# Kernel tuning notes

Hardware: AMD Instinct MI355X
Metric: run time of the kernel (lower is better)

The kernel has to match this reference:

```python
import jax, jax.numpy as jnp
import numpy as np

SPATIAL_SCALE = 0.125  # stride-8 FPN level
POINTS = 5


def _sample_points(bb):
    # bb: [N,H,W,5] = (cx, cy, w, h, theta) in image coords
    cx, cy, w, h, t = [bb[..., i] for i in range(5)]
    if POINTS == 1:
        px = cx[..., None]
        py = cy[..., None]
    else:
        vx = w * jnp.cos(t) * 0.5
        vy = w * jnp.sin(t) * 0.5
        wx = -h * jnp.sin(t) * 0.5
        wy = h * jnp.cos(t) * 0.5
        px = jnp.stack([cx, cx + vx + wx, cx - vx + wx, cx - vx - wx, cx + vx - wx], axis=-1)
        py = jnp.stack([cy, cy + vy + wy, cy - vy + wy, cy - vy - wy, cy + vy - wy], axis=-1)
    return px * SPATIAL_SCALE, py * SPATIAL_SCALE  # [N,H,W,P] feature-map coords


def _bilinear_gather(feat, y, x):
    # feat: [N,C,H,W]; y,x: [N,H,W,P] -> [N,H,W,P,C], mmcv-style bilinear w/ border rules
    N, C, H, W = feat.shape
    valid = (y >= -1.0) & (y <= H) & (x >= -1.0) & (x <= W)
    y = jnp.maximum(y, 0.0)
    x = jnp.maximum(x, 0.0)
    y_low = jnp.minimum(jnp.floor(y).astype(jnp.int32), H - 1)
    x_low = jnp.minimum(jnp.floor(x).astype(jnp.int32), W - 1)
    # if low index hits last row/col, snap coordinate onto it (ly/lx = 0)
    y = jnp.where(y_low >= H - 1, y_low.astype(feat.dtype), y)
    x = jnp.where(x_low >= W - 1, x_low.astype(feat.dtype), x)
    y_high = jnp.minimum(y_low + 1, H - 1)
    x_high = jnp.minimum(x_low + 1, W - 1)
    ly = y - y_low.astype(feat.dtype)
    lx = x - x_low.astype(feat.dtype)
    hy = 1.0 - ly
    hx = 1.0 - lx
    nn = jnp.arange(N)[:, None, None, None]  # broadcasts against [N,H,W,P]

    def g(yy, xx):
        return feat[nn, :, yy, xx]  # [N,H,W,P,C]

    val = ((hy * hx)[..., None] * g(y_low, x_low)
           + (hy * lx)[..., None] * g(y_low, x_high)
           + (ly * hx)[..., None] * g(y_high, x_low)
           + (ly * lx)[..., None] * g(y_high, x_high))
    return jnp.where(valid[..., None], val, 0.0)


def feature_refine(features, best_rbboxes):
    px, py = _sample_points(best_rbboxes)
    sampled = _bilinear_gather(features, py, px)       # [N,H,W,P,C]
    acc = sampled.sum(axis=3)                           # [N,H,W,C]
    return features + jnp.transpose(acc, (0, 3, 1, 2))  # [N,C,H,W]


def setup_inputs() -> dict:
    key = jax.random.key(0)
    k1, k2, k3, k4, k5, k6 = jax.random.split(key, 6)
    N, C, H, W = 4, 256, 128, 128
    IMG = 1024.0
    features = jax.random.normal(k1, (N, C, H, W), dtype=jnp.float32)
    cx = jax.random.uniform(k2, (N, H, W), minval=0.0, maxval=IMG)
    cy = jax.random.uniform(k3, (N, H, W), minval=0.0, maxval=IMG)
    bw = jax.random.uniform(k4, (N, H, W), minval=8.0, maxval=128.0)
    bh = jax.random.uniform(k5, (N, H, W), minval=8.0, maxval=128.0)
    th = jax.random.uniform(k6, (N, H, W), minval=-np.pi / 2, maxval=np.pi / 2)
    best_rbboxes = jnp.stack([cx, cy, bw, bh, th], axis=-1)  # [N,H,W,5]
    return {"features": features, "best_rbboxes": best_rbboxes}


def reference(features, best_rbboxes):
    return feature_refine(features, best_rbboxes)
```

## Files before the change

### kernel.cpp

```cpp
#include <hip/hip_runtime.h>


#define N_ 4
#define C_ 256
#define H_ 128
#define W_ 128
#define HW_ (H_ * W_)
#define SCALE 0.125f

typedef unsigned int uint32;

__device__ __forceinline__ uint32 f2bf(float f) {
    uint32 u = __float_as_uint(f);
    u = (u + 0x7FFF + ((u >> 16) & 1)) >> 16;
    return u;
}
__device__ __forceinline__ float blo(uint32 u) { return __uint_as_float(u << 16); }
__device__ __forceinline__ float bhi(uint32 u) { return __uint_as_float(u & 0xFFFF0000u); }

__global__ __launch_bounds__(256) void geo_kernel(const float* __restrict__ bb,
                                                  uint32* __restrict__ geoG)
{
    const int px = blockIdx.x * 256 + threadIdx.x;
    const float* b = bb + (size_t)px * 5;
    const float cx = b[0], cy = b[1], bw = b[2], bh = b[3], th = b[4];
    const float st = sinf(th), ct = cosf(th);
    const float vx = bw * ct * 0.5f, vy = bw * st * 0.5f;
    const float wx = -bh * st * 0.5f, wy = bh * ct * 0.5f;
    const float pxs[5] = {cx, cx + vx + wx, cx - vx + wx, cx - vx - wx, cx + vx - wx};
    const float pys[5] = {cy, cy + vy + wy, cy - vy + wy, cy - vy - wy, cy + vy - wy};

    uint32* g = geoG + (size_t)px * 32;
#pragma unroll
    for (int p = 0; p < 5; ++p) {
        float x = pxs[p] * SCALE;
        float y = pys[p] * SCALE;
        const bool valid = (y >= -1.0f) && (y <= (float)H_) &&
                           (x >= -1.0f) && (x <= (float)W_);
        y = fmaxf(y, 0.0f);
        x = fmaxf(x, 0.0f);
        int yl = min((int)y, H_ - 1);
        int xl = min((int)x, W_ - 1);
        if (yl >= H_ - 1) y = (float)yl;
        if (xl >= W_ - 1) x = (float)xl;
        const int yh = min(yl + 1, H_ - 1);
        const float ly = y - (float)yl, lx = x - (float)xl;
        const float hy = 1.0f - ly,     hx = 1.0f - lx;
        const int xa = min(xl, W_ - 2);
        float wA, wB;
        if (xl < W_ - 1) { wA = hx; wB = lx; }
        else             { wA = 0.0f; wB = 1.0f; }
        const float v = valid ? 1.0f : 0.0f;
        g[p]      = (uint32)(yl * W_ + xa);
        g[5 + p]  = (uint32)(yh * W_ + xa);
        g[10 + p] = __float_as_uint(v * hy * wA);
        g[15 + p] = __float_as_uint(v * hy * wB);
        g[20 + p] = __float_as_uint(v * ly * wA);
        g[25 + p] = __float_as_uint(v * ly * wB);
    }
    g[30] = 0u; g[31] = 0u;
}

__global__ __launch_bounds__(512) void nchw2nhwc_bf16(const float* __restrict__ in,
                                                      uint32* __restrict__ outU)
{
    __shared__ uint32 tile[128 * 130];
    const int t   = threadIdx.x;
    const int l   = t & 63;
    const int g   = t >> 6;
    const int hw0 = blockIdx.x * 128;
    const int n   = blockIdx.y;
    const float* base = in + (size_t)n * C_ * HW_ + hw0;
#pragma unroll 4
    for (int i = 0; i < 16; ++i) {
        const int cp = i * 8 + g;
        const int c  = cp * 2;
        const float2 v0 = *(const float2*)(base + (size_t)c * HW_ + 2 * l);
        const float2 v1 = *(const float2*)(base + (size_t)(c + 1) * HW_ + 2 * l);
        tile[(2 * l) * 130 + cp]     = f2bf(v0.x) | (f2bf(v1.x) << 16);
        tile[(2 * l + 1) * 130 + cp] = f2bf(v0.y) | (f2bf(v1.y) << 16);
    }
    __syncthreads();
#pragma unroll 4
    for (int i = 0; i < 16; ++i) {
        const int r = i * 8 + g;
        const uint2 v = *(const uint2*)&tile[r * 130 + 2 * l];
        *(uint2*)(outU + ((size_t)n * HW_ + hw0 + r) * 128 + 2 * l) = v;
    }
}

__global__ __launch_bounds__(256) void fr_refine(const uint32* __restrict__ nhwcU,
                                                 const uint32* __restrict__ geoG,
                                                 float* __restrict__ out)
{
    __shared__ float tile[32 * 260];
    const int t  = threadIdx.x;
    const int l  = t & 63;
    const int wv = __builtin_amdgcn_readfirstlane(t >> 6);
    const int bx = blockIdx.x;
    const int xcd = bx & 7;
    const int n   = xcd >> 1;
    const int idx = ((bx >> 3) << 1) | (xcd & 1);
    const int h   = idx >> 2;
    const int w0  = (idx & 3) * 32;

    const float idsel = (l < 32) ? 1.0f : 0.0f;
    const uint32* plane = nhwcU + (size_t)n * HW_ * 128;
    const uint32* gb = geoG + (size_t)((n * H_ + h) * W_ + w0 + wv * 8) * 32;

#pragma unroll 2
    for (int p = 0; p < 8; ++p) {
        const uint32* g = gb + p * 32;
        const int hwp = h * W_ + w0 + wv * 8 + p;

        float a[8];
        {
            const uint4 r = *(const uint4*)(plane + (size_t)hwp * 128 + 4 * l);
            a[0] = idsel * blo(r.x); a[1] = idsel * bhi(r.x);
            a[2] = idsel * blo(r.y); a[3] = idsel * bhi(r.y);
            a[4] = idsel * blo(r.z); a[5] = idsel * bhi(r.z);
            a[6] = idsel * blo(r.w); a[7] = idsel * bhi(r.w);
        }
#pragma unroll
        for (int q = 0; q < 5; ++q) {
            const int o0 = (int)g[q];
            const int o1 = (int)g[5 + q];
            const float w00 = __uint_as_float(g[10 + q]);
            const float w01 = __uint_as_float(g[15 + q]);
            const float w10 = __uint_as_float(g[20 + q]);
            const float w11 = __uint_as_float(g[25 + q]);
            const float wr0 = (l < 32) ? w00 : w01;
            const float wr1 = (l < 32) ? w10 : w11;
            const uint4 r0 = *(const uint4*)(plane + (size_t)o0 * 128 + 4 * l);
            const uint4 r1 = *(const uint4*)(plane + (size_t)o1 * 128 + 4 * l);
            a[0] = fmaf(wr0, blo(r0.x), a[0]); a[1] = fmaf(wr0, bhi(r0.x), a[1]);
            a[2] = fmaf(wr0, blo(r0.y), a[2]); a[3] = fmaf(wr0, bhi(r0.y), a[3]);
            a[4] = fmaf(wr0, blo(r0.z), a[4]); a[5] = fmaf(wr0, bhi(r0.z), a[5]);
            a[6] = fmaf(wr0, blo(r0.w), a[6]); a[7] = fmaf(wr0, bhi(r0.w), a[7]);
            a[0] = fmaf(wr1, blo(r1.x), a[0]); a[1] = fmaf(wr1, bhi(r1.x), a[1]);
            a[2] = fmaf(wr1, blo(r1.y), a[2]); a[3] = fmaf(wr1, bhi(r1.y), a[3]);
            a[4] = fmaf(wr1, blo(r1.z), a[4]); a[5] = fmaf(wr1, bhi(r1.z), a[5]);
            a[6] = fmaf(wr1, blo(r1.w), a[6]); a[7] = fmaf(wr1, bhi(r1.w), a[7]);
        }
#pragma unroll
        for (int k = 0; k < 8; ++k) a[k] += __shfl_xor(a[k], 32, 64);
        if (l < 32) {
            const int pxl = wv * 8 + p;
            float* dst = &tile[pxl * 260 + 8 * l];
            *(float4*)dst       = make_float4(a[0], a[1], a[2], a[3]);
            *(float4*)(dst + 4) = make_float4(a[4], a[5], a[6], a[7]);
        }
    }
    __syncthreads();
    const size_t obase = (size_t)n * C_ * HW_ + h * W_ + w0;
#pragma unroll 4
    for (int it = 0; it < 32; ++it) {
        const int flat = it * 256 + t;
        const int px = flat & 31;
        const int c  = flat >> 5;
        out[obase + (size_t)c * HW_ + px] = tile[px * 260 + c];
    }
}

__global__ __launch_bounds__(256) void fr_kernel(
    const float* __restrict__ feat,
    const float* __restrict__ bb,
    float* __restrict__ out)
{
    const int lane = threadIdx.x & 63;
    const int wave = threadIdx.x >> 6;
    const int tile = blockIdx.x;
    const int wt   = tile & 1;
    const int h    = (tile >> 1) & (H_ - 1);
    const int n    = tile >> 8;
    const int w    = wt * 64 + lane;
    const int cb   = blockIdx.y;

    const float* b = bb + (size_t)((n * H_ + h) * W_ + w) * 5;
    const float cx = b[0], cy = b[1], bw = b[2], bh = b[3], th = b[4];
    const float st = sinf(th), ct = cosf(th);
    const float vx = bw * ct * 0.5f, vy = bw * st * 0.5f;
    const float wx = -bh * st * 0.5f, wy = bh * ct * 0.5f;
    const float pxs[5] = {cx, cx + vx + wx, cx - vx + wx, cx - vx - wx, cx + vx - wx};
    const float pys[5] = {cy, cy + vy + wy, cy - vy + wy, cy - vy - wy, cy + vy - wy};

    int   off0[5], off1[5];
    float wgt[20];
#pragma unroll
    for (int p = 0; p < 5; ++p) {
        float x = pxs[p] * SCALE;
        float y = pys[p] * SCALE;
        const bool valid = (y >= -1.0f) && (y <= (float)H_) &&
                           (x >= -1.0f) && (x <= (float)W_);
        y = fmaxf(y, 0.0f);
        x = fmaxf(x, 0.0f);
        int yl = min((int)y, H_ - 1);
        int xl = min((int)x, W_ - 1);
        if (yl >= H_ - 1) y = (float)yl;
        if (xl >= W_ - 1) x = (float)xl;
        const int yh = min(yl + 1, H_ - 1);
        const float ly = y - (float)yl, lx = x - (float)xl;
        const float hy = 1.0f - ly,     hx = 1.0f - lx;
        const int xa = min(xl, W_ - 2);
        float wA, wB;
        if (xl < W_ - 1) { wA = hx; wB = lx; }
        else             { wA = 0.0f; wB = 1.0f; }
        const float v = valid ? 1.0f : 0.0f;
        off0[p] = yl * W_ + xa;
        off1[p] = yh * W_ + xa;
        wgt[p * 4 + 0] = v * hy * wA;
        wgt[p * 4 + 1] = v * hy * wB;
        wgt[p * 4 + 2] = v * ly * wA;
        wgt[p * 4 + 3] = v * ly * wB;
    }

    const int hw = h * W_ + w;
    const size_t planeBase = ((size_t)n * C_ + cb * 64 + wave * 16) * HW_;
    const float* fp = feat + planeBase;
    float*       op = out  + planeBase;
    for (int it = 0; it < 16; ++it) {
        float acc = fp[hw];
#pragma unroll
        for (int p = 0; p < 5; ++p) {
            acc += wgt[p * 4 + 0] * fp[off0[p]]
                 + wgt[p * 4 + 1] * fp[off0[p] + 1]
                 + wgt[p * 4 + 2] * fp[off1[p]]
                 + wgt[p * 4 + 3] * fp[off1[p] + 1];
        }
        op[hw] = acc;
        fp += HW_;
        op += HW_;
    }
}

extern "C" void kernel_launch(void* const* d_in, const int* in_sizes, int n_in,
                              void* d_out, int out_size, void* d_ws, size_t ws_size,
                              hipStream_t stream) {
    const float* feat = (const float*)d_in[0];
    const float* bbox = (const float*)d_in[1];
    float* out = (float*)d_out;

    const size_t nhwcBytes = (size_t)N_ * HW_ * C_ * 2;
    const size_t geoBytes  = (size_t)N_ * HW_ * 32 * 4;
    if (ws_size >= nhwcBytes + geoBytes) {
        uint32* nhwcU = (uint32*)d_ws;
        uint32* geoG  = (uint32*)((char*)d_ws + nhwcBytes);
        geo_kernel<<<dim3(N_ * HW_ / 256), dim3(256), 0, stream>>>(bbox, geoG);
        nchw2nhwc_bf16<<<dim3(HW_ / 128, N_), dim3(512), 0, stream>>>(feat, nhwcU);
        fr_refine<<<dim3(N_ * H_ * (W_ / 32)), dim3(256), 0, stream>>>(nhwcU, geoG, out);
    } else {
        dim3 grid(N_ * H_ * (W_ / 64), C_ / 64, 1);
        fr_kernel<<<grid, dim3(256), 0, stream>>>(feat, bbox, out);
    }
}
```

Before: 179.1 us.

## Widen NCHW-to-NHWC bf16 transpose to float4 loads and remap refine block order

The transpose kernel now handles 256 spatial positions per 1024-thread block. It uses float4 global loads batched eight per thread and uint4 shared-memory writes laid out channel-major, then writes the output as fully contiguous dwords. The goal is fewer, wider global memory transactions and more loads in flight. Separately, the refine kernel's block-to-(h,w) mapping changes so that each XCD pair covers contiguous halves of the image rather than interleaved rows, which may improve L2 locality for neighbouring gathers. The new transpose uses about 130KB of LDS and strided LDS reads (stride 260), which may cause bank conflicts and lower occupancy.

```diff
diff --git a/kernel.cpp b/kernel.cpp
--- a/kernel.cpp
+++ b/kernel.cpp
@@ -61,31 +61,45 @@
     g[30] = 0u; g[31] = 0u;
 }
 
-__global__ __launch_bounds__(512) void nchw2nhwc_bf16(const float* __restrict__ in,
-                                                      uint32* __restrict__ outU)
-{
-    __shared__ uint32 tile[128 * 130];
+__global__ __launch_bounds__(1024) void nchw2nhwc_bf16(const float* __restrict__ in,
+                                                       uint32* __restrict__ outU)
+{
+    __shared__ uint32 tile[128 * 260];
     const int t   = threadIdx.x;
     const int l   = t & 63;
     const int g   = t >> 6;
-    const int hw0 = blockIdx.x * 128;
+    const int hw0 = blockIdx.x * 256;
     const int n   = blockIdx.y;
-    const float* base = in + (size_t)n * C_ * HW_ + hw0;
-#pragma unroll 4
-    for (int i = 0; i < 16; ++i) {
-        const int cp = i * 8 + g;
-        const int c  = cp * 2;
-        const float2 v0 = *(const float2*)(base + (size_t)c * HW_ + 2 * l);
-        const float2 v1 = *(const float2*)(base + (size_t)(c + 1) * HW_ + 2 * l);
-        tile[(2 * l) * 130 + cp]     = f2bf(v0.x) | (f2bf(v1.x) << 16);
-        tile[(2 * l + 1) * 130 + cp] = f2bf(v0.y) | (f2bf(v1.y) << 16);
+    const float* base = in + (size_t)n * C_ * HW_ + hw0 + 4 * l;
+
+#pragma unroll
+    for (int half = 0; half < 2; ++half) {
+        float4 v0[4], v1[4];
+#pragma unroll
+        for (int r = 0; r < 4; ++r) {
+            const int cp = g * 8 + half * 4 + r;
+            v0[r] = *(const float4*)(base + (size_t)(2 * cp) * HW_);
+            v1[r] = *(const float4*)(base + (size_t)(2 * cp + 1) * HW_);
+        }
+#pragma unroll
+        for (int r = 0; r < 4; ++r) {
+            const int cp = g * 8 + half * 4 + r;
+            uint4 u;
+            u.x = f2bf(v0[r].x) | (f2bf(v1[r].x) << 16);
+            u.y = f2bf(v0[r].y) | (f2bf(v1[r].y) << 16);
+            u.z = f2bf(v0[r].z) | (f2bf(v1[r].z) << 16);
+            u.w = f2bf(v0[r].w) | (f2bf(v1[r].w) << 16);
+            *(uint4*)&tile[cp * 260 + 4 * l] = u;
+        }
     }
     __syncthreads();
-#pragma unroll 4
-    for (int i = 0; i < 16; ++i) {
-        const int r = i * 8 + g;
-        const uint2 v = *(const uint2*)&tile[r * 130 + 2 * l];
-        *(uint2*)(outU + ((size_t)n * HW_ + hw0 + r) * 128 + 2 * l) = v;
+    uint32* dst = outU + ((size_t)n * HW_ + hw0) * 128;
+#pragma unroll 8
+    for (int it = 0; it < 32; ++it) {
+        const int f   = it * 1024 + t;
+        const int row = f >> 7;
+        const int q   = f & 127;
+        dst[f] = tile[q * 260 + row];
     }
 }
 
@@ -100,9 +114,9 @@
     const int bx = blockIdx.x;
     const int xcd = bx & 7;
     const int n   = xcd >> 1;
-    const int idx = ((bx >> 3) << 1) | (xcd & 1);
-    const int h   = idx >> 2;
-    const int w0  = (idx & 3) * 32;
+    const int s   = bx >> 3;
+    const int h   = ((xcd & 1) << 6) | (s >> 2);
+    const int w0  = (s & 3) * 32;
 
     const float idsel = (l < 32) ? 1.0f : 0.0f;
     const uint32* plane = nhwcU + (size_t)n * HW_ * 128;
@@ -246,7 +260,7 @@
         uint32* nhwcU = (uint32*)d_ws;
         uint32* geoG  = (uint32*)((char*)d_ws + nhwcBytes);
         geo_kernel<<<dim3(N_ * HW_ / 256), dim3(256), 0, stream>>>(bbox, geoG);
-        nchw2nhwc_bf16<<<dim3(HW_ / 128, N_), dim3(512), 0, stream>>>(feat, nhwcU);
+        nchw2nhwc_bf16<<<dim3(HW_ / 256, N_), dim3(1024), 0, stream>>>(feat, nhwcU);
         fr_refine<<<dim3(N_ * H_ * (W_ / 32)), dim3(256), 0, stream>>>(nhwcU, geoG, out);
     } else {
         dim3 grid(N_ * H_ * (W_ / 64), C_ / 64, 1);
```

Result: faster. 175.5 us (-2.0%).
